# Optimization experiments

Hardware: AMD Instinct MI355X
Metric: run time of the kernel (lower is better)

Reference implementation:

```python
import jax, jax.numpy as jnp
import numpy as np

N_NODES = 50000
N_EDGES = 800000
DIM = 128
N_LAYERS = 5
BN_EPS = 1e-3  # keras BatchNormalization default epsilon


def setup_inputs() -> dict:
    key = jax.random.key(0)
    ks = jax.random.split(key, 6)
    scale = 1.0 / np.sqrt(DIM)
    return {
        "x": jax.random.normal(ks[0], (N_NODES, DIM), dtype=jnp.float32),
        "edge_src": jax.random.randint(ks[1], (N_EDGES,), 0, N_NODES, dtype=jnp.int32),
        "edge_dst": jax.random.randint(ks[2], (N_EDGES,), 0, N_NODES, dtype=jnp.int32),
        "eps": jnp.zeros((N_LAYERS,), dtype=jnp.float32),
        "W1": jax.random.normal(ks[3], (N_LAYERS, DIM, DIM), dtype=jnp.float32) * scale,
        "b1": jnp.zeros((N_LAYERS, DIM), dtype=jnp.float32),
        "W2": jax.random.normal(ks[4], (N_LAYERS, DIM, DIM), dtype=jnp.float32) * scale,
        "b2": jnp.zeros((N_LAYERS, DIM), dtype=jnp.float32),
        "gamma": jnp.ones((N_LAYERS, DIM), dtype=jnp.float32),
        "beta": jnp.zeros((N_LAYERS, DIM), dtype=jnp.float32),
        "bn_mean": jnp.zeros((N_LAYERS, DIM), dtype=jnp.float32),
        "bn_var": jnp.ones((N_LAYERS, DIM), dtype=jnp.float32),
    }


def reference(x, edge_src, edge_dst, eps, W1, b1, W2, b2, gamma, beta, bn_mean, bn_var):
    n = x.shape[0]
    num_layers = W1.shape[0]
    hidden_rep = [x]
    h = x
    for l in range(num_layers):
        # sparse Adj @ h as gather + segment-sum (sum neighbor pooling)
        msgs = jnp.take(h, edge_src, axis=0)                       # [E, D]
        pooled = jax.ops.segment_sum(msgs, edge_dst, num_segments=n)  # [N, D]
        pooled = pooled + (1.0 + eps[l]) * h                        # GIN eps term
        # 2-layer MLP: Linear -> ReLU -> Linear
        z = jax.nn.relu(pooled @ W1[l] + b1[l])
        z = z @ W2[l] + b2[l]
        # BatchNorm (inference: moving statistics)
        z = gamma[l] * (z - bn_mean[l]) * jax.lax.rsqrt(bn_var[l] + BN_EPS) + beta[l]
        h = jax.nn.relu(z)
        hidden_rep.append(h)
    return tuple(hidden_rep)
```

## Files before the change

### kernel.cpp

```cpp
#include <hip/hip_runtime.h>
#include <hip/hip_bf16.h>

#define N_NODES 50000
#define N_EDGES 800000
#define DIM 128
#define N_LAYERS 5
#define BN_EPS 1e-3f

typedef __attribute__((ext_vector_type(8))) short bf16x8;
typedef __attribute__((ext_vector_type(4))) float f32x4;

__device__ __forceinline__ unsigned short f2bf(float f) {
    unsigned int v = __builtin_bit_cast(unsigned int, f);
    v += 0x7fffu + ((v >> 16) & 1u);
    return (unsigned short)(v >> 16);
}
__device__ __forceinline__ float bflo(unsigned int v) {
    return __builtin_bit_cast(float, v << 16);
}
__device__ __forceinline__ float bfhi(unsigned int v) {
    return __builtin_bit_cast(float, v & 0xffff0000u);
}


__global__ void init_x_kernel(const float* __restrict__ x, float* __restrict__ out,
                              unsigned short* __restrict__ hb) {
    int t = blockIdx.x * blockDim.x + threadIdx.x;
    if (t >= (N_NODES * DIM) / 4) return;
    float4 v = ((const float4*)x)[t];
    ((float4*)out)[t] = v;
    unsigned short u[4] = {f2bf(v.x), f2bf(v.y), f2bf(v.z), f2bf(v.w)};
    *(uint2*)(hb + t * 4) = *(uint2*)u;
}

__global__ void zero_i32_kernel(int* __restrict__ p, int n) {
    int t = blockIdx.x * blockDim.x + threadIdx.x;
    if (t < n) p[t] = 0;
}

__global__ void hist_kernel(const int* __restrict__ dst, int* __restrict__ cnt) {
    int e = blockIdx.x * blockDim.x + threadIdx.x;
    if (e < N_EDGES) atomicAdd(&cnt[dst[e]], 1);
}

__global__ __launch_bounds__(1024) void scan_kernel(const int* __restrict__ cnt,
                                                    int* __restrict__ row_start,
                                                    int* __restrict__ cursor) {
    __shared__ int wsum[16];
    __shared__ int s_carry;
    const int tid = threadIdx.x;
    const int lane = tid & 63, wave = tid >> 6;
    if (tid == 0) s_carry = 0;
    __syncthreads();
    for (int base = 0; base < N_NODES; base += 4096) {
        int i0 = base + tid * 4;
        int v[4];
#pragma unroll
        for (int j = 0; j < 4; j++) {
            int i = i0 + j;
            v[j] = (i < N_NODES) ? cnt[i] : 0;
        }
        int s = v[0] + v[1] + v[2] + v[3];
        int x = s;
#pragma unroll
        for (int off = 1; off < 64; off <<= 1) {
            int t = __shfl_up(x, off, 64);
            if (lane >= off) x += t;
        }
        if (lane == 63) wsum[wave] = x;
        __syncthreads();
        if (wave == 0) {
            int w = (lane < 16) ? wsum[lane] : 0;
#pragma unroll
            for (int off = 1; off < 16; off <<= 1) {
                int t = __shfl_up(w, off, 64);
                if (lane >= off) w += t;
            }
            if (lane < 16) wsum[lane] = w;
        }
        __syncthreads();
        int waveoff = (wave > 0) ? wsum[wave - 1] : 0;
        int carry = s_carry;
        int run = carry + waveoff + (x - s);
#pragma unroll
        for (int j = 0; j < 4; j++) {
            int i = i0 + j;
            if (i < N_NODES) { row_start[i] = run; cursor[i] = run; }
            run += v[j];
        }
        __syncthreads();
        if (tid == 1023) s_carry = carry + wsum[15];
        __syncthreads();
    }
    if (tid == 0) row_start[N_NODES] = s_carry;
}

__global__ void fill_kernel(const int* __restrict__ src, const int* __restrict__ dst,
                            int* __restrict__ cursor, int* __restrict__ col) {
    int e = blockIdx.x * blockDim.x + threadIdx.x;
    if (e < N_EDGES) {
        int d = dst[e];
        int pos = atomicAdd(&cursor[d], 1);
        col[pos] = src[e];
    }
}

__global__ void pack_w_kernel(const float* __restrict__ W1,
                              const float* __restrict__ W2,
                              unsigned short* __restrict__ wp) {
    int t = blockIdx.x * blockDim.x + threadIdx.x;
    if (t >= N_LAYERS * 2 * 2048) return;
    int mat = t >> 11;
    int r = t & 2047;
    int ks = r >> 9, nt = (r >> 6) & 7, lane = r & 63;
    int layer = mat >> 1;
    const float* W = ((mat & 1) ? W2 : W1) + layer * DIM * DIM;
    int n = nt * 16 + (lane & 15);
    int kb = ks * 32 + (lane >> 4) * 8;
    unsigned short u[8];
#pragma unroll
    for (int j = 0; j < 8; j++) u[j] = f2bf(W[(kb + j) * DIM + n]);
    *(uint4*)(wp + (size_t)mat * 16384 + ((ks * 8 + nt) * 64 + lane) * 8) = *(uint4*)u;
}

__global__ void bn_prep_kernel(const float* __restrict__ gamma,
                               const float* __restrict__ beta,
                               const float* __restrict__ mean,
                               const float* __restrict__ var,
                               float* __restrict__ scale, float* __restrict__ shift) {
    int i = blockIdx.x * blockDim.x + threadIdx.x;
    if (i < N_LAYERS * DIM) {
        float sc = gamma[i] * rsqrtf(var[i] + BN_EPS);
        scale[i] = sc;
        shift[i] = beta[i] - mean[i] * sc;
    }
}


__global__ __launch_bounds__(256) void pool_kernel(const unsigned short* __restrict__ hb,
                                                   const int* __restrict__ row_start,
                                                   const int* __restrict__ col,
                                                   const float* __restrict__ eps_l,
                                                   unsigned short* __restrict__ pooled_b) {
    const int wave = threadIdx.x >> 6, lane = threadIdx.x & 63;
    const int n = blockIdx.x * 4 + wave;
    if (n >= N_NODES) return;
    const float ev = 1.0f + eps_l[0];
    const int s0 = row_start[n], s1 = row_start[n + 1];

    unsigned int sv = *(const unsigned int*)(hb + n * DIM + lane * 2);
    float a0 = ev * bflo(sv);
    float a1 = ev * bfhi(sv);

    for (int base = s0; base < s1; base += 64) {
        const int nn = s1 - base < 64 ? s1 - base : 64;
        int ci = (base + lane < s1) ? col[base + lane] : 0;
        int j = 0;
        for (; j + 1 < nn; j += 2) {
            int sa = __shfl(ci, j, 64);
            int sb = __shfl(ci, j + 1, 64);
            unsigned int va = *(const unsigned int*)(hb + sa * DIM + lane * 2);
            unsigned int vb = *(const unsigned int*)(hb + sb * DIM + lane * 2);
            a0 += bflo(va); a1 += bfhi(va);
            a0 += bflo(vb); a1 += bfhi(vb);
        }
        if (j < nn) {
            int sa = __shfl(ci, j, 64);
            unsigned int va = *(const unsigned int*)(hb + sa * DIM + lane * 2);
            a0 += bflo(va); a1 += bfhi(va);
        }
    }
    unsigned short u[2] = {f2bf(a0), f2bf(a1)};
    *(unsigned int*)(pooled_b + n * DIM + lane * 2) = *(unsigned int*)u;
}

__global__ __launch_bounds__(256) void mlp_kernel(
    const unsigned short* __restrict__ pooled_b,
    const unsigned short* __restrict__ wp1,
    const unsigned short* __restrict__ wp2,
    const float* __restrict__ b1,
    const float* __restrict__ b2,
    const float* __restrict__ bnscale,
    const float* __restrict__ bnshift,
    float* __restrict__ h_out,
    unsigned short* __restrict__ hb_out) {
    __shared__ __align__(16) unsigned short zfrag[4][4][64][8];
    const int tid = threadIdx.x;
    const int wave = tid >> 6, lane = tid & 63;
    const int m0 = blockIdx.x * 64;
    const int colc = lane & 15;
    const int quad = lane >> 4;
    const int arow = m0 + wave * 16 + colc;
    const int arow_c = arow < N_NODES ? arow : N_NODES - 1;

    bf16x8 a[4];
#pragma unroll
    for (int ks = 0; ks < 4; ks++)
        a[ks] = *(const bf16x8*)(pooled_b + arow_c * DIM + ks * 32 + quad * 8);

    f32x4 acc[8];
#pragma unroll
    for (int nt = 0; nt < 8; nt++) {
        acc[nt] = (f32x4){0.f, 0.f, 0.f, 0.f};
#pragma unroll
        for (int ks = 0; ks < 4; ks++) {
            bf16x8 b = *(const bf16x8*)(wp1 + ((ks * 8 + nt) * 64 + lane) * 8);
            acc[nt] = __builtin_amdgcn_mfma_f32_16x16x32_bf16(a[ks], b, acc[nt], 0, 0, 0);
        }
    }

#pragma unroll
    for (int nt = 0; nt < 8; nt++) {
        int n = nt * 16 + colc;
        float bias = b1[n];
#pragma unroll
        for (int r = 0; r < 4; r++) {
            float v = acc[nt][r] + bias;
            v = v > 0.f ? v : 0.f;
            int row16 = quad * 4 + r;
            zfrag[wave][n >> 5][(((n >> 3) & 3) << 4) | row16][n & 7] = f2bf(v);
        }
    }

#pragma unroll
    for (int ks = 0; ks < 4; ks++) a[ks] = *(const bf16x8*)(&zfrag[wave][ks][lane][0]);

    f32x4 acc2[8];
#pragma unroll
    for (int nt = 0; nt < 8; nt++) {
        acc2[nt] = (f32x4){0.f, 0.f, 0.f, 0.f};
#pragma unroll
        for (int ks = 0; ks < 4; ks++) {
            bf16x8 b = *(const bf16x8*)(wp2 + ((ks * 8 + nt) * 64 + lane) * 8);
            acc2[nt] = __builtin_amdgcn_mfma_f32_16x16x32_bf16(a[ks], b, acc2[nt], 0, 0, 0);
        }
    }

#pragma unroll
    for (int nt = 0; nt < 8; nt++) {
        int n = nt * 16 + colc;
        float bias = b2[n];
        float sc = bnscale[n], sh = bnshift[n];
#pragma unroll
        for (int r = 0; r < 4; r++) {
            int row = m0 + wave * 16 + quad * 4 + r;
            if (row < N_NODES) {
                float z = acc2[nt][r] + bias;
                z = z * sc + sh;
                z = z > 0.f ? z : 0.f;
                h_out[row * DIM + n] = z;
                hb_out[row * DIM + n] = f2bf(z);
            }
        }
    }
}


extern "C" void kernel_launch(void* const* d_in, const int* in_sizes, int n_in,
                              void* d_out, int out_size, void* d_ws, size_t ws_size,
                              hipStream_t stream) {
    const float* x     = (const float*)d_in[0];
    const int* esrc    = (const int*)d_in[1];
    const int* edst    = (const int*)d_in[2];
    const float* eps   = (const float*)d_in[3];
    const float* W1    = (const float*)d_in[4];
    const float* b1    = (const float*)d_in[5];
    const float* W2    = (const float*)d_in[6];
    const float* b2    = (const float*)d_in[7];
    const float* gam   = (const float*)d_in[8];
    const float* bet   = (const float*)d_in[9];
    const float* bmean = (const float*)d_in[10];
    const float* bvar  = (const float*)d_in[11];
    float* out = (float*)d_out;

    char* ws = (char*)d_ws;
    unsigned short* hb       = (unsigned short*)(ws);
    unsigned short* pooled_b = (unsigned short*)(ws + 12800000);
    int*   col        = (int*)  (ws + 25600000);
    int*   row_start  = (int*)  (ws + 28800000);
    int*   cursor     = (int*)  (ws + 29000008);
    int*   cnt        = (int*)  (ws + 29200008);
    unsigned short* wpack = (unsigned short*)(ws + 29400008);
    float* bnscale    = (float*)(ws + 29727688);
    float* bnshift    = (float*)(ws + 29730248);

    init_x_kernel<<<6250, 256, 0, stream>>>(x, out, hb);
    zero_i32_kernel<<<(N_NODES + 255) / 256, 256, 0, stream>>>(cnt, N_NODES);
    hist_kernel<<<(N_EDGES + 255) / 256, 256, 0, stream>>>(edst, cnt);
    scan_kernel<<<1, 1024, 0, stream>>>(cnt, row_start, cursor);
    fill_kernel<<<(N_EDGES + 255) / 256, 256, 0, stream>>>(esrc, edst, cursor, col);
    pack_w_kernel<<<(N_LAYERS * 2 * 2048 + 255) / 256, 256, 0, stream>>>(W1, W2, wpack);
    bn_prep_kernel<<<(N_LAYERS * DIM + 255) / 256, 256, 0, stream>>>(gam, bet, bmean, bvar,
                                                                     bnscale, bnshift);

    const int pool_blocks = (N_NODES + 3) / 4;
    const int mlp_blocks  = (N_NODES + 63) / 64;
    for (int l = 0; l < N_LAYERS; l++) {
        float* h_next = out + (size_t)(l + 1) * N_NODES * DIM;
        pool_kernel<<<pool_blocks, 256, 0, stream>>>(hb, row_start, col, eps + l, pooled_b);
        mlp_kernel<<<mlp_blocks, 256, 0, stream>>>(
            pooled_b,
            wpack + (size_t)(l * 2) * 16384,
            wpack + (size_t)(l * 2 + 1) * 16384,
            b1 + l * DIM, b2 + l * DIM,
            bnscale + l * DIM, bnshift + l * DIM,
            h_next, hb);
    }
}
```

Before: 630.6 us.

## Fuse neighbor pooling into MLP kernel with ping-pong bf16 buffers

Merges the gather/segment-sum pooling kernel into the MLP kernel. Each wave pools its 16 rows straight into LDS fragments, so the pooled bf16 round trip through global memory and one launch per layer go away. The hidden state now ping-pongs between two bf16 buffers, and the gather loop is unrolled by 8 for more loads in flight. The setup kernels are also merged to cut launches. The risk is lower parallelism in the gather phase: only 782 blocks, with each wave doing 16 nodes serially, instead of one node per wave across 12500 blocks. This could hurt latency hiding on the irregular gather.

```diff
diff --git a/kernel.cpp b/kernel.cpp
--- a/kernel.cpp
+++ b/kernel.cpp
@@ -23,19 +23,17 @@
 }
 
 
-__global__ void init_x_kernel(const float* __restrict__ x, float* __restrict__ out,
-                              unsigned short* __restrict__ hb) {
+__global__ void init_zero_kernel(const float* __restrict__ x, float* __restrict__ out,
+                                 unsigned short* __restrict__ hb, int* __restrict__ cnt) {
     int t = blockIdx.x * blockDim.x + threadIdx.x;
-    if (t >= (N_NODES * DIM) / 4) return;
-    float4 v = ((const float4*)x)[t];
-    ((float4*)out)[t] = v;
-    unsigned short u[4] = {f2bf(v.x), f2bf(v.y), f2bf(v.z), f2bf(v.w)};
-    *(uint2*)(hb + t * 4) = *(uint2*)u;
-}
-
-__global__ void zero_i32_kernel(int* __restrict__ p, int n) {
-    int t = blockIdx.x * blockDim.x + threadIdx.x;
-    if (t < n) p[t] = 0;
+    if (t < (N_NODES * DIM) / 4) {
+        float4 v = ((const float4*)x)[t];
+        ((float4*)out)[t] = v;
+        unsigned short u[4] = {f2bf(v.x), f2bf(v.y), f2bf(v.z), f2bf(v.w)};
+        *(uint2*)(hb + t * 4) = *(uint2*)u;
+    }
+    int z = t - (N_NODES * DIM) / 4;
+    if (z >= 0 && z < N_NODES) cnt[z] = 0;
 }
 
 __global__ void hist_kernel(const int* __restrict__ dst, int* __restrict__ cnt) {
@@ -105,77 +103,38 @@
     }
 }
 
-__global__ void pack_w_kernel(const float* __restrict__ W1,
-                              const float* __restrict__ W2,
-                              unsigned short* __restrict__ wp) {
+__global__ void prep_kernel(const float* __restrict__ W1, const float* __restrict__ W2,
+                            unsigned short* __restrict__ wp,
+                            const float* __restrict__ gamma, const float* __restrict__ beta,
+                            const float* __restrict__ mean, const float* __restrict__ var,
+                            float* __restrict__ scale, float* __restrict__ shift) {
     int t = blockIdx.x * blockDim.x + threadIdx.x;
-    if (t >= N_LAYERS * 2 * 2048) return;
-    int mat = t >> 11;
-    int r = t & 2047;
-    int ks = r >> 9, nt = (r >> 6) & 7, lane = r & 63;
-    int layer = mat >> 1;
-    const float* W = ((mat & 1) ? W2 : W1) + layer * DIM * DIM;
-    int n = nt * 16 + (lane & 15);
-    int kb = ks * 32 + (lane >> 4) * 8;
-    unsigned short u[8];
-#pragma unroll
-    for (int j = 0; j < 8; j++) u[j] = f2bf(W[(kb + j) * DIM + n]);
-    *(uint4*)(wp + (size_t)mat * 16384 + ((ks * 8 + nt) * 64 + lane) * 8) = *(uint4*)u;
-}
-
-__global__ void bn_prep_kernel(const float* __restrict__ gamma,
-                               const float* __restrict__ beta,
-                               const float* __restrict__ mean,
-                               const float* __restrict__ var,
-                               float* __restrict__ scale, float* __restrict__ shift) {
-    int i = blockIdx.x * blockDim.x + threadIdx.x;
-    if (i < N_LAYERS * DIM) {
+    if (t < N_LAYERS * 2 * 2048) {
+        int mat = t >> 11;
+        int r = t & 2047;
+        int ks = r >> 9, nt = (r >> 6) & 7, lane = r & 63;
+        int layer = mat >> 1;
+        const float* W = ((mat & 1) ? W2 : W1) + layer * DIM * DIM;
+        int n = nt * 16 + (lane & 15);
+        int kb = ks * 32 + (lane >> 4) * 8;
+        unsigned short u[8];
+#pragma unroll
+        for (int j = 0; j < 8; j++) u[j] = f2bf(W[(kb + j) * DIM + n]);
+        *(uint4*)(wp + (size_t)mat * 16384 + ((ks * 8 + nt) * 64 + lane) * 8) = *(uint4*)u;
+    }
+    int i = t - N_LAYERS * 2 * 2048;
+    if (i >= 0 && i < N_LAYERS * DIM) {
         float sc = gamma[i] * rsqrtf(var[i] + BN_EPS);
         scale[i] = sc;
         shift[i] = beta[i] - mean[i] * sc;
     }
 }
 
-
-__global__ __launch_bounds__(256) void pool_kernel(const unsigned short* __restrict__ hb,
-                                                   const int* __restrict__ row_start,
-                                                   const int* __restrict__ col,
-                                                   const float* __restrict__ eps_l,
-                                                   unsigned short* __restrict__ pooled_b) {
-    const int wave = threadIdx.x >> 6, lane = threadIdx.x & 63;
-    const int n = blockIdx.x * 4 + wave;
-    if (n >= N_NODES) return;
-    const float ev = 1.0f + eps_l[0];
-    const int s0 = row_start[n], s1 = row_start[n + 1];
-
-    unsigned int sv = *(const unsigned int*)(hb + n * DIM + lane * 2);
-    float a0 = ev * bflo(sv);
-    float a1 = ev * bfhi(sv);
-
-    for (int base = s0; base < s1; base += 64) {
-        const int nn = s1 - base < 64 ? s1 - base : 64;
-        int ci = (base + lane < s1) ? col[base + lane] : 0;
-        int j = 0;
-        for (; j + 1 < nn; j += 2) {
-            int sa = __shfl(ci, j, 64);
-            int sb = __shfl(ci, j + 1, 64);
-            unsigned int va = *(const unsigned int*)(hb + sa * DIM + lane * 2);
-            unsigned int vb = *(const unsigned int*)(hb + sb * DIM + lane * 2);
-            a0 += bflo(va); a1 += bfhi(va);
-            a0 += bflo(vb); a1 += bfhi(vb);
-        }
-        if (j < nn) {
-            int sa = __shfl(ci, j, 64);
-            unsigned int va = *(const unsigned int*)(hb + sa * DIM + lane * 2);
-            a0 += bflo(va); a1 += bfhi(va);
-        }
-    }
-    unsigned short u[2] = {f2bf(a0), f2bf(a1)};
-    *(unsigned int*)(pooled_b + n * DIM + lane * 2) = *(unsigned int*)u;
-}
-
-__global__ __launch_bounds__(256) void mlp_kernel(
-    const unsigned short* __restrict__ pooled_b,
+__global__ __launch_bounds__(256) void layer_kernel(
+    const unsigned short* __restrict__ hb_in,
+    const int* __restrict__ row_start,
+    const int* __restrict__ col,
+    const float* __restrict__ eps_l,
     const unsigned short* __restrict__ wp1,
     const unsigned short* __restrict__ wp2,
     const float* __restrict__ b1,
@@ -184,19 +143,51 @@
     const float* __restrict__ bnshift,
     float* __restrict__ h_out,
     unsigned short* __restrict__ hb_out) {
-    __shared__ __align__(16) unsigned short zfrag[4][4][64][8];
+    __shared__ __align__(16) unsigned short afrag[4][4][64][8];
     const int tid = threadIdx.x;
     const int wave = tid >> 6, lane = tid & 63;
-    const int m0 = blockIdx.x * 64;
-    const int colc = lane & 15;
-    const int quad = lane >> 4;
-    const int arow = m0 + wave * 16 + colc;
-    const int arow_c = arow < N_NODES ? arow : N_NODES - 1;
+    const int m0 = blockIdx.x * 64 + wave * 16;
+    const float ev = 1.0f + eps_l[0];
+    const int c = lane * 2;
+    const int ks_w = c >> 5, idx_w = (((c >> 3) & 3) << 4), j_w = c & 7;
+
+    for (int r = 0; r < 16; r++) {
+        const int n = m0 + r;
+        float a0 = 0.f, a1 = 0.f;
+        if (n < N_NODES) {
+            unsigned int sv = *(const unsigned int*)(hb_in + n * DIM + c);
+            a0 = ev * bflo(sv);
+            a1 = ev * bfhi(sv);
+            const int s0 = row_start[n], s1 = row_start[n + 1];
+            for (int base = s0; base < s1; base += 64) {
+                const int nn = (s1 - base < 64) ? (s1 - base) : 64;
+                int ci = (base + lane < s1) ? col[base + lane] : 0;
+                int j = 0;
+                for (; j + 7 < nn; j += 8) {
+                    int s[8];
+                    unsigned int v[8];
+#pragma unroll
+                    for (int q = 0; q < 8; q++) s[q] = __shfl(ci, j + q, 64);
+#pragma unroll
+                    for (int q = 0; q < 8; q++)
+                        v[q] = *(const unsigned int*)(hb_in + s[q] * DIM + c);
+#pragma unroll
+                    for (int q = 0; q < 8; q++) { a0 += bflo(v[q]); a1 += bfhi(v[q]); }
+                }
+                for (; j < nn; j++) {
+                    int sq = __shfl(ci, j, 64);
+                    unsigned int vq = *(const unsigned int*)(hb_in + sq * DIM + c);
+                    a0 += bflo(vq); a1 += bfhi(vq);
+                }
+            }
+        }
+        unsigned short u[2] = {f2bf(a0), f2bf(a1)};
+        *(unsigned int*)&afrag[wave][ks_w][idx_w | r][j_w] = *(unsigned int*)u;
+    }
 
     bf16x8 a[4];
 #pragma unroll
-    for (int ks = 0; ks < 4; ks++)
-        a[ks] = *(const bf16x8*)(pooled_b + arow_c * DIM + ks * 32 + quad * 8);
+    for (int ks = 0; ks < 4; ks++) a[ks] = *(const bf16x8*)(&afrag[wave][ks][lane][0]);
 
     f32x4 acc[8];
 #pragma unroll
@@ -209,6 +200,8 @@
         }
     }
 
+    const int colc = lane & 15;
+    const int quad = lane >> 4;
 #pragma unroll
     for (int nt = 0; nt < 8; nt++) {
         int n = nt * 16 + colc;
@@ -218,12 +211,12 @@
             float v = acc[nt][r] + bias;
             v = v > 0.f ? v : 0.f;
             int row16 = quad * 4 + r;
-            zfrag[wave][n >> 5][(((n >> 3) & 3) << 4) | row16][n & 7] = f2bf(v);
-        }
-    }
-
-#pragma unroll
-    for (int ks = 0; ks < 4; ks++) a[ks] = *(const bf16x8*)(&zfrag[wave][ks][lane][0]);
+            afrag[wave][n >> 5][(((n >> 3) & 3) << 4) | row16][n & 7] = f2bf(v);
+        }
+    }
+
+#pragma unroll
+    for (int ks = 0; ks < 4; ks++) a[ks] = *(const bf16x8*)(&afrag[wave][ks][lane][0]);
 
     f32x4 acc2[8];
 #pragma unroll
@@ -243,7 +236,7 @@
         float sc = bnscale[n], sh = bnshift[n];
 #pragma unroll
         for (int r = 0; r < 4; r++) {
-            int row = m0 + wave * 16 + quad * 4 + r;
+            int row = m0 + quad * 4 + r;
             if (row < N_NODES) {
                 float z = acc2[nt][r] + bias;
                 z = z * sc + sh;
@@ -274,8 +267,8 @@
     float* out = (float*)d_out;
 
     char* ws = (char*)d_ws;
-    unsigned short* hb       = (unsigned short*)(ws);
-    unsigned short* pooled_b = (unsigned short*)(ws + 12800000);
+    unsigned short* hb0   = (unsigned short*)(ws);
+    unsigned short* hb1   = (unsigned short*)(ws + 12800000);
     int*   col        = (int*)  (ws + 25600000);
     int*   row_start  = (int*)  (ws + 28800000);
     int*   cursor     = (int*)  (ws + 29000008);
@@ -284,26 +277,24 @@
     float* bnscale    = (float*)(ws + 29727688);
     float* bnshift    = (float*)(ws + 29730248);
 
-    init_x_kernel<<<6250, 256, 0, stream>>>(x, out, hb);
-    zero_i32_kernel<<<(N_NODES + 255) / 256, 256, 0, stream>>>(cnt, N_NODES);
+    init_zero_kernel<<<((N_NODES * DIM) / 4 + N_NODES + 255) / 256, 256, 0, stream>>>(
+        x, out, hb0, cnt);
     hist_kernel<<<(N_EDGES + 255) / 256, 256, 0, stream>>>(edst, cnt);
     scan_kernel<<<1, 1024, 0, stream>>>(cnt, row_start, cursor);
     fill_kernel<<<(N_EDGES + 255) / 256, 256, 0, stream>>>(esrc, edst, cursor, col);
-    pack_w_kernel<<<(N_LAYERS * 2 * 2048 + 255) / 256, 256, 0, stream>>>(W1, W2, wpack);
-    bn_prep_kernel<<<(N_LAYERS * DIM + 255) / 256, 256, 0, stream>>>(gam, bet, bmean, bvar,
-                                                                     bnscale, bnshift);
-
-    const int pool_blocks = (N_NODES + 3) / 4;
-    const int mlp_blocks  = (N_NODES + 63) / 64;
+    prep_kernel<<<(N_LAYERS * 2 * 2048 + N_LAYERS * DIM + 255) / 256, 256, 0, stream>>>(
+        W1, W2, wpack, gam, bet, bmean, bvar, bnscale, bnshift);
+
+    const int blocks = (N_NODES + 63) / 64;
+    unsigned short* hbuf[2] = {hb0, hb1};
     for (int l = 0; l < N_LAYERS; l++) {
         float* h_next = out + (size_t)(l + 1) * N_NODES * DIM;
-        pool_kernel<<<pool_blocks, 256, 0, stream>>>(hb, row_start, col, eps + l, pooled_b);
-        mlp_kernel<<<mlp_blocks, 256, 0, stream>>>(
-            pooled_b,
+        layer_kernel<<<blocks, 256, 0, stream>>>(
+            hbuf[l & 1], row_start, col, eps + l,
             wpack + (size_t)(l * 2) * 16384,
             wpack + (size_t)(l * 2 + 1) * 16384,
             b1 + l * DIM, b2 + l * DIM,
             bnscale + l * DIM, bnshift + l * DIM,
-            h_next, hb);
-    }
-}
+            h_next, hbuf[(l + 1) & 1]);
+    }
+}
```

Result: slower. 815.1 us (+29.3%).
